# Performance work log

Measured on AMD Instinct MI355X. Metric: run time of the kernel, lower is better.

## Reference

```python
import jax, jax.numpy as jnp
import numpy as np

B, D, K = 32768, 1024, 64
N3, N4, N5 = 512, 512, 512


def setup_inputs() -> dict:
    key = jax.random.key(0)
    ks = jax.random.split(key, 10)
    # x in [-1, 1]^D as the docstring states
    x = jax.random.uniform(ks[0], (B, D), dtype=jnp.float32, minval=-1.0, maxval=1.0)
    S = jnp.sort(jax.random.randint(ks[1], (K,), 0, D, dtype=jnp.int32))
    a = jax.random.normal(ks[2], (K,), dtype=jnp.float32)
    b = jax.random.normal(ks[3], (K, K), dtype=jnp.float32)
    idx3 = jax.random.randint(ks[4], (N3, 3), 0, K, dtype=jnp.int32)
    c3 = jax.random.normal(ks[5], (N3,), dtype=jnp.float32)
    idx4 = jax.random.randint(ks[6], (N4, 4), 0, K, dtype=jnp.int32)
    c4 = jax.random.normal(ks[7], (N4,), dtype=jnp.float32)
    idx5 = jax.random.randint(ks[8], (N5, 5), 0, K, dtype=jnp.int32)
    c5 = jax.random.normal(ks[9], (N5,), dtype=jnp.float32)
    return {"x": x, "S": S, "a": a, "b": b, "idx3": idx3, "c3": c3,
            "idx4": idx4, "c4": c4, "idx5": idx5, "c5": c5}


def _monomial_term(xS, idx, c):
    # xS: (B,k); idx: (n,deg); c: (n,) -> (B,)
    # gather -> (B, n, deg), product over monomial factors, weighted sum
    prod = jnp.prod(xS[:, idx], axis=2)  # (B, n)
    return prod @ c


def reference(x, S, a, b, idx3, c3, idx4, c4, idx5, c5):
    xS = x[:, S]                      # (B, k)
    lin = xS @ a                      # (B,)
    # sum_{i<j} b[i,j] xS_i xS_j == einsum with strictly-upper-triangular b
    bu = jnp.triu(b, k=1)             # (k, k)
    quad = jnp.einsum('bi,ij,bj->b', xS, bu, xS)
    out = lin + quad
    out = out + _monomial_term(xS, idx3, c3)
    out = out + _monomial_term(xS, idx4, c4)
    out = out + _monomial_term(xS, idx5, c5)
    return out
```

## Files before the change

### kernel.cpp

```cpp
#include <hip/hip_runtime.h>
#include <stdint.h>

#define NT 256
#define RPB 16
#define XSTR 80

#define WS_P3   0
#define WS_P4   4096
#define WS_P5   12288
#define WS_BUT  20480

static __device__ __forceinline__ unsigned short f2bf(float f) {
    unsigned u = __float_as_uint(f);
    return (unsigned short)((u + 0x7FFFu + ((u >> 16) & 1u)) >> 16);
}
static __device__ __forceinline__ float bfbits(unsigned lo16) {
    return __uint_as_float(lo16 << 16);
}
static __device__ __forceinline__ float4 f4fma(float s, float4 v, float4 acc) {
    acc.x += s * v.x; acc.y += s * v.y; acc.z += s * v.z; acc.w += s * v.w;
    return acc;
}

__global__ void prepack(const float* __restrict__ b,
                        const int* __restrict__ i3, const float* __restrict__ c3,
                        const int* __restrict__ i4, const float* __restrict__ c4,
                        const int* __restrict__ i5, const float* __restrict__ c5,
                        unsigned char* __restrict__ ws)
{
    const int g = blockIdx.x * NT + threadIdx.x;
    float* buT = (float*)(ws + WS_BUT);
    if (g < 4096) {
        int j = g >> 6, i = g & 63;
        buT[g] = (i < j) ? b[i * 64 + j] : 0.0f;
    }
    if (g < 512) {
        unsigned o0, o1, o2, o3, o4;
        o0 = (unsigned)i3[3*g+0] * XSTR; o1 = (unsigned)i3[3*g+1] * XSTR; o2 = (unsigned)i3[3*g+2] * XSTR;
        ((uint2*)(ws + WS_P3))[g] = make_uint2(o0 | (o1 << 16), o2 | ((unsigned)f2bf(c3[g]) << 16));
        o0 = (unsigned)i4[4*g+0] * XSTR; o1 = (unsigned)i4[4*g+1] * XSTR;
        o2 = (unsigned)i4[4*g+2] * XSTR; o3 = (unsigned)i4[4*g+3] * XSTR;
        ((uint4*)(ws + WS_P4))[g] = make_uint4(o0 | (o1 << 16), o2 | (o3 << 16), (unsigned)f2bf(c4[g]), 0u);
        o0 = (unsigned)i5[5*g+0] * XSTR; o1 = (unsigned)i5[5*g+1] * XSTR;
        o2 = (unsigned)i5[5*g+2] * XSTR; o3 = (unsigned)i5[5*g+3] * XSTR;
        o4 = (unsigned)i5[5*g+4] * XSTR;
        ((uint4*)(ws + WS_P5))[g] = make_uint4(o0 | (o1 << 16), o2 | (o3 << 16), o4 | ((unsigned)f2bf(c5[g]) << 16), 0u);
    }
}

__global__ __launch_bounds__(NT, 4)
void poly_main(const float* __restrict__ x, const int* __restrict__ S,
               const float* __restrict__ a,
               const unsigned char* __restrict__ ws, float* __restrict__ out)
{
    __shared__ __align__(16) float xS[64 * 20];
    __shared__ float red[64];

    const int tid  = threadIdx.x;
    const int row0 = blockIdx.x * RPB;

    {
        const int k = tid & 63, q = tid >> 6;
        const int sk = S[k];
        const float* xc = x + (size_t)row0 * 1024 + sk;
        #pragma unroll
        for (int m = 0; m < 4; ++m) {
            int r = q * 4 + m;
            xS[k * 20 + r] = xc[(size_t)r * 1024];
        }
    }
    __syncthreads();

    const int rg = tid & 3;
    const int ts = tid >> 2;
    const char* xb = (const char*)xS + rg * 16;

    float4 d = make_float4(0.f, 0.f, 0.f, 0.f);
    {
        const float4* buT4 = (const float4*)(ws + WS_BUT) + ts * 16;
        const int nii = (ts + 3) >> 2;
        #pragma unroll 4
        for (int ii = 0; ii < nii; ++ii) {
            float4 bb  = buT4[ii];
            float4 xi0 = *(const float4*)(xb + (ii * 4 + 0) * XSTR);
            float4 xi1 = *(const float4*)(xb + (ii * 4 + 1) * XSTR);
            float4 xi2 = *(const float4*)(xb + (ii * 4 + 2) * XSTR);
            float4 xi3 = *(const float4*)(xb + (ii * 4 + 3) * XSTR);
            d = f4fma(bb.x, xi0, d);
            d = f4fma(bb.y, xi1, d);
            d = f4fma(bb.z, xi2, d);
            d = f4fma(bb.w, xi3, d);
        }
    }
    const float av = a[ts];
    float4 xj = *(const float4*)(xb + ts * XSTR);
    float4 acc;
    acc.x = (av + d.x) * xj.x;
    acc.y = (av + d.y) * xj.y;
    acc.z = (av + d.z) * xj.z;
    acc.w = (av + d.w) * xj.w;

    const uint2* p3 = (const uint2*)(ws + WS_P3);
    const uint4* p4 = (const uint4*)(ws + WS_P4);
    const uint4* p5 = (const uint4*)(ws + WS_P5);

    #pragma unroll 4
    for (int m = 0; m < 8; ++m) {
        uint2 p = p3[64 * m + ts];
        float4 v0 = *(const float4*)(xb + (p.x & 0xFFFFu));
        float4 v1 = *(const float4*)(xb + (p.x >> 16));
        float4 v2 = *(const float4*)(xb + (p.y & 0xFFFFu));
        float c = bfbits(p.y >> 16);
        acc.x += c * ((v0.x * v1.x) * v2.x);
        acc.y += c * ((v0.y * v1.y) * v2.y);
        acc.z += c * ((v0.z * v1.z) * v2.z);
        acc.w += c * ((v0.w * v1.w) * v2.w);
    }
    #pragma unroll 4
    for (int m = 0; m < 8; ++m) {
        uint4 p = p4[64 * m + ts];
        float4 v0 = *(const float4*)(xb + (p.x & 0xFFFFu));
        float4 v1 = *(const float4*)(xb + (p.x >> 16));
        float4 v2 = *(const float4*)(xb + (p.y & 0xFFFFu));
        float4 v3 = *(const float4*)(xb + (p.y >> 16));
        float c = bfbits(p.z & 0xFFFFu);
        acc.x += c * ((v0.x * v1.x) * (v2.x * v3.x));
        acc.y += c * ((v0.y * v1.y) * (v2.y * v3.y));
        acc.z += c * ((v0.z * v1.z) * (v2.z * v3.z));
        acc.w += c * ((v0.w * v1.w) * (v2.w * v3.w));
    }
    #pragma unroll 4
    for (int m = 0; m < 8; ++m) {
        uint4 p = p5[64 * m + ts];
        float4 v0 = *(const float4*)(xb + (p.x & 0xFFFFu));
        float4 v1 = *(const float4*)(xb + (p.x >> 16));
        float4 v2 = *(const float4*)(xb + (p.y & 0xFFFFu));
        float4 v3 = *(const float4*)(xb + (p.y >> 16));
        float4 v4 = *(const float4*)(xb + (p.z & 0xFFFFu));
        float c = bfbits(p.z >> 16);
        acc.x += c * (((v0.x * v1.x) * (v2.x * v3.x)) * v4.x);
        acc.y += c * (((v0.y * v1.y) * (v2.y * v3.y)) * v4.y);
        acc.z += c * (((v0.z * v1.z) * (v2.z * v3.z)) * v4.z);
        acc.w += c * (((v0.w * v1.w) * (v2.w * v3.w)) * v4.w);
    }

    #pragma unroll
    for (int mask = 4; mask <= 32; mask <<= 1) {
        acc.x += __shfl_xor(acc.x, mask, 64);
        acc.y += __shfl_xor(acc.y, mask, 64);
        acc.z += __shfl_xor(acc.z, mask, 64);
        acc.w += __shfl_xor(acc.w, mask, 64);
    }
    const int w = tid >> 6, lane = tid & 63;
    if (lane < 4) ((float4*)red)[w * 4 + lane] = acc;
    __syncthreads();
    if (tid < 16) {
        out[row0 + tid] = red[tid] + red[16 + tid] + red[32 + tid] + red[48 + tid];
    }
}

extern "C" void kernel_launch(void* const* d_in, const int* in_sizes, int n_in,
                              void* d_out, int out_size, void* d_ws, size_t ws_size,
                              hipStream_t stream) {
    const float* x  = (const float*)d_in[0];
    const int*   S  = (const int*)d_in[1];
    const float* a  = (const float*)d_in[2];
    const float* b  = (const float*)d_in[3];
    const int*   i3 = (const int*)d_in[4];
    const float* c3 = (const float*)d_in[5];
    const int*   i4 = (const int*)d_in[6];
    const float* c4 = (const float*)d_in[7];
    const int*   i5 = (const int*)d_in[8];
    const float* c5 = (const float*)d_in[9];
    unsigned char* ws = (unsigned char*)d_ws;
    float* out = (float*)d_out;

    prepack<<<16, NT, 0, stream>>>(b, i3, c3, i4, c4, i5, c5, ws);
    poly_main<<<32768 / RPB, NT, 0, stream>>>(x, S, a, ws, out);
}
```

Measured before the change: 213.3 us.

## Switch gathered features and monomial math to packed fp16 with 32 rows per block

Gathered x values, the triangular b matrix and the monomial coefficients are now stored as fp16, and the quadratic and monomial products are computed with packed half2 FMA/mul, with 8 rows per thread group instead of 4 floats. Rows per block double to 32, so the same LDS row stride holds twice as many rows and each instruction does twice the work. This halves LDS traffic and ALU instruction count per row. The cost is a large precision loss: fp16 accumulation over about 1600 terms with normal-distributed coefficients may overflow or exceed tolerance.

```diff
diff --git a/kernel.cpp b/kernel.cpp
--- a/kernel.cpp
+++ b/kernel.cpp
@@ -1,25 +1,22 @@
 #include <hip/hip_runtime.h>
+#include <hip/hip_fp16.h>
 #include <stdint.h>
 
 #define NT 256
-#define RPB 16
+#define RPB 32
 #define XSTR 80
 
 #define WS_P3   0
 #define WS_P4   4096
 #define WS_P5   12288
-#define WS_BUT  20480
-
-static __device__ __forceinline__ unsigned short f2bf(float f) {
-    unsigned u = __float_as_uint(f);
-    return (unsigned short)((u + 0x7FFFu + ((u >> 16) & 1u)) >> 16);
-}
-static __device__ __forceinline__ float bfbits(unsigned lo16) {
-    return __uint_as_float(lo16 << 16);
-}
-static __device__ __forceinline__ float4 f4fma(float s, float4 v, float4 acc) {
-    acc.x += s * v.x; acc.y += s * v.y; acc.z += s * v.z; acc.w += s * v.w;
-    return acc;
+#define WS_BUTH 20480
+
+static __device__ __forceinline__ __half2 H2(unsigned u) {
+    return __builtin_bit_cast(__half2, u);
+}
+static __device__ __forceinline__ unsigned short f2hbits(float f) {
+    __half h = __float2half(f);
+    return __builtin_bit_cast(unsigned short, h);
 }
 
 __global__ void prepack(const float* __restrict__ b,
@@ -29,23 +26,42 @@
                         unsigned char* __restrict__ ws)
 {
     const int g = blockIdx.x * NT + threadIdx.x;
-    float* buT = (float*)(ws + WS_BUT);
     if (g < 4096) {
         int j = g >> 6, i = g & 63;
-        buT[g] = (i < j) ? b[i * 64 + j] : 0.0f;
+        float v = (i < j) ? b[i * 64 + j] : 0.0f;
+        ((unsigned short*)(ws + WS_BUTH))[g] = f2hbits(v);
     }
     if (g < 512) {
         unsigned o0, o1, o2, o3, o4;
         o0 = (unsigned)i3[3*g+0] * XSTR; o1 = (unsigned)i3[3*g+1] * XSTR; o2 = (unsigned)i3[3*g+2] * XSTR;
-        ((uint2*)(ws + WS_P3))[g] = make_uint2(o0 | (o1 << 16), o2 | ((unsigned)f2bf(c3[g]) << 16));
+        ((uint2*)(ws + WS_P3))[g] = make_uint2(o0 | (o1 << 16), o2 | ((unsigned)f2hbits(c3[g]) << 16));
         o0 = (unsigned)i4[4*g+0] * XSTR; o1 = (unsigned)i4[4*g+1] * XSTR;
         o2 = (unsigned)i4[4*g+2] * XSTR; o3 = (unsigned)i4[4*g+3] * XSTR;
-        ((uint4*)(ws + WS_P4))[g] = make_uint4(o0 | (o1 << 16), o2 | (o3 << 16), (unsigned)f2bf(c4[g]), 0u);
+        ((uint4*)(ws + WS_P4))[g] = make_uint4(o0 | (o1 << 16), o2 | (o3 << 16), (unsigned)f2hbits(c4[g]), 0u);
         o0 = (unsigned)i5[5*g+0] * XSTR; o1 = (unsigned)i5[5*g+1] * XSTR;
         o2 = (unsigned)i5[5*g+2] * XSTR; o3 = (unsigned)i5[5*g+3] * XSTR;
         o4 = (unsigned)i5[5*g+4] * XSTR;
-        ((uint4*)(ws + WS_P5))[g] = make_uint4(o0 | (o1 << 16), o2 | (o3 << 16), o4 | ((unsigned)f2bf(c5[g]) << 16), 0u);
-    }
+        ((uint4*)(ws + WS_P5))[g] = make_uint4(o0 | (o1 << 16), o2 | (o3 << 16), o4 | ((unsigned)f2hbits(c5[g]) << 16), 0u);
+    }
+}
+
+static __device__ __forceinline__ void qfma(__half2 bb, uint4 xk, __half2 d[4]) {
+    d[0] = __hfma2(bb, H2(xk.x), d[0]);
+    d[1] = __hfma2(bb, H2(xk.y), d[1]);
+    d[2] = __hfma2(bb, H2(xk.z), d[2]);
+    d[3] = __hfma2(bb, H2(xk.w), d[3]);
+}
+static __device__ __forceinline__ void pmul(const uint4& a, __half2 p[4]) {
+    p[0] = __hmul2(p[0], H2(a.x));
+    p[1] = __hmul2(p[1], H2(a.y));
+    p[2] = __hmul2(p[2], H2(a.z));
+    p[3] = __hmul2(p[3], H2(a.w));
+}
+static __device__ __forceinline__ void pacc(__half2 c2, const __half2 p[4], __half2 acc[4]) {
+    acc[0] = __hfma2(c2, p[0], acc[0]);
+    acc[1] = __hfma2(c2, p[1], acc[1]);
+    acc[2] = __hfma2(c2, p[2], acc[2]);
+    acc[3] = __hfma2(c2, p[3], acc[3]);
 }
 
 __global__ __launch_bounds__(NT, 4)
@@ -53,8 +69,8 @@
                const float* __restrict__ a,
                const unsigned char* __restrict__ ws, float* __restrict__ out)
 {
-    __shared__ __align__(16) float xS[64 * 20];
-    __shared__ float red[64];
+    __shared__ __align__(16) __half xS[64 * 40];
+    __shared__ float red[4][4][8];
 
     const int tid  = threadIdx.x;
     const int row0 = blockIdx.x * RPB;
@@ -63,11 +79,15 @@
         const int k = tid & 63, q = tid >> 6;
         const int sk = S[k];
         const float* xc = x + (size_t)row0 * 1024 + sk;
+        float v[8];
         #pragma unroll
-        for (int m = 0; m < 4; ++m) {
-            int r = q * 4 + m;
-            xS[k * 20 + r] = xc[(size_t)r * 1024];
-        }
+        for (int m = 0; m < 8; ++m) v[m] = xc[(size_t)(q * 8 + m) * 1024];
+        uint4 pk;
+        pk.x = __builtin_bit_cast(unsigned, __floats2half2_rn(v[0], v[1]));
+        pk.y = __builtin_bit_cast(unsigned, __floats2half2_rn(v[2], v[3]));
+        pk.z = __builtin_bit_cast(unsigned, __floats2half2_rn(v[4], v[5]));
+        pk.w = __builtin_bit_cast(unsigned, __floats2half2_rn(v[6], v[7]));
+        *(uint4*)((char*)xS + k * XSTR + q * 16) = pk;
     }
     __syncthreads();
 
@@ -75,30 +95,35 @@
     const int ts = tid >> 2;
     const char* xb = (const char*)xS + rg * 16;
 
-    float4 d = make_float4(0.f, 0.f, 0.f, 0.f);
+    __half2 d[4] = {H2(0u), H2(0u), H2(0u), H2(0u)};
     {
-        const float4* buT4 = (const float4*)(ws + WS_BUT) + ts * 16;
-        const int nii = (ts + 3) >> 2;
-        #pragma unroll 4
-        for (int ii = 0; ii < nii; ++ii) {
-            float4 bb  = buT4[ii];
-            float4 xi0 = *(const float4*)(xb + (ii * 4 + 0) * XSTR);
-            float4 xi1 = *(const float4*)(xb + (ii * 4 + 1) * XSTR);
-            float4 xi2 = *(const float4*)(xb + (ii * 4 + 2) * XSTR);
-            float4 xi3 = *(const float4*)(xb + (ii * 4 + 3) * XSTR);
-            d = f4fma(bb.x, xi0, d);
-            d = f4fma(bb.y, xi1, d);
-            d = f4fma(bb.z, xi2, d);
-            d = f4fma(bb.w, xi3, d);
+        const uint4* buTh4 = (const uint4*)(ws + WS_BUTH) + ts * 8;
+        const int nii = (ts + 7) >> 3;
+        #pragma unroll 2
+        for (int g = 0; g < nii; ++g) {
+            uint4 bw = buTh4[g];
+            const char* xkb = xb + g * 8 * XSTR;
+            unsigned pw[4] = {bw.x, bw.y, bw.z, bw.w};
+            #pragma unroll
+            for (int p = 0; p < 4; ++p) {
+                __half2 blo = __half2half2(__ushort_as_half((unsigned short)(pw[p] & 0xFFFFu)));
+                __half2 bhi = __half2half2(__ushort_as_half((unsigned short)(pw[p] >> 16)));
+                uint4 x0 = *(const uint4*)(xkb + (2 * p + 0) * XSTR);
+                uint4 x1 = *(const uint4*)(xkb + (2 * p + 1) * XSTR);
+                qfma(blo, x0, d);
+                qfma(bhi, x1, d);
+            }
         }
     }
-    const float av = a[ts];
-    float4 xj = *(const float4*)(xb + ts * XSTR);
-    float4 acc;
-    acc.x = (av + d.x) * xj.x;
-    acc.y = (av + d.y) * xj.y;
-    acc.z = (av + d.z) * xj.z;
-    acc.w = (av + d.w) * xj.w;
+    __half2 acc[4];
+    {
+        __half2 a2 = __half2half2(__float2half(a[ts]));
+        uint4 xj = *(const uint4*)(xb + ts * XSTR);
+        acc[0] = __hmul2(__hadd2(a2, d[0]), H2(xj.x));
+        acc[1] = __hmul2(__hadd2(a2, d[1]), H2(xj.y));
+        acc[2] = __hmul2(__hadd2(a2, d[2]), H2(xj.z));
+        acc[3] = __hmul2(__hadd2(a2, d[3]), H2(xj.w));
+    }
 
     const uint2* p3 = (const uint2*)(ws + WS_P3);
     const uint4* p4 = (const uint4*)(ws + WS_P4);
@@ -107,55 +132,63 @@
     #pragma unroll 4
     for (int m = 0; m < 8; ++m) {
         uint2 p = p3[64 * m + ts];
-        float4 v0 = *(const float4*)(xb + (p.x & 0xFFFFu));
-        float4 v1 = *(const float4*)(xb + (p.x >> 16));
-        float4 v2 = *(const float4*)(xb + (p.y & 0xFFFFu));
-        float c = bfbits(p.y >> 16);
-        acc.x += c * ((v0.x * v1.x) * v2.x);
-        acc.y += c * ((v0.y * v1.y) * v2.y);
-        acc.z += c * ((v0.z * v1.z) * v2.z);
-        acc.w += c * ((v0.w * v1.w) * v2.w);
-    }
-    #pragma unroll 4
+        uint4 v0 = *(const uint4*)(xb + (p.x & 0xFFFFu));
+        uint4 v1 = *(const uint4*)(xb + (p.x >> 16));
+        uint4 v2 = *(const uint4*)(xb + (p.y & 0xFFFFu));
+        __half2 pr[4] = {H2(v0.x), H2(v0.y), H2(v0.z), H2(v0.w)};
+        pmul(v1, pr);
+        pmul(v2, pr);
+        pacc(__half2half2(__ushort_as_half((unsigned short)(p.y >> 16))), pr, acc);
+    }
+    #pragma unroll 2
     for (int m = 0; m < 8; ++m) {
         uint4 p = p4[64 * m + ts];
-        float4 v0 = *(const float4*)(xb + (p.x & 0xFFFFu));
-        float4 v1 = *(const float4*)(xb + (p.x >> 16));
-        float4 v2 = *(const float4*)(xb + (p.y & 0xFFFFu));
-        float4 v3 = *(const float4*)(xb + (p.y >> 16));
-        float c = bfbits(p.z & 0xFFFFu);
-        acc.x += c * ((v0.x * v1.x) * (v2.x * v3.x));
-        acc.y += c * ((v0.y * v1.y) * (v2.y * v3.y));
-        acc.z += c * ((v0.z * v1.z) * (v2.z * v3.z));
-        acc.w += c * ((v0.w * v1.w) * (v2.w * v3.w));
-    }
-    #pragma unroll 4
+        uint4 v0 = *(const uint4*)(xb + (p.x & 0xFFFFu));
+        uint4 v1 = *(const uint4*)(xb + (p.x >> 16));
+        uint4 v2 = *(const uint4*)(xb + (p.y & 0xFFFFu));
+        uint4 v3 = *(const uint4*)(xb + (p.y >> 16));
+        __half2 pr[4] = {H2(v0.x), H2(v0.y), H2(v0.z), H2(v0.w)};
+        pmul(v1, pr);
+        pmul(v2, pr);
+        pmul(v3, pr);
+        pacc(__half2half2(__ushort_as_half((unsigned short)(p.z & 0xFFFFu))), pr, acc);
+    }
+    #pragma unroll 2
     for (int m = 0; m < 8; ++m) {
         uint4 p = p5[64 * m + ts];
-        float4 v0 = *(const float4*)(xb + (p.x & 0xFFFFu));
-        float4 v1 = *(const float4*)(xb + (p.x >> 16));
-        float4 v2 = *(const float4*)(xb + (p.y & 0xFFFFu));
-        float4 v3 = *(const float4*)(xb + (p.y >> 16));
-        float4 v4 = *(const float4*)(xb + (p.z & 0xFFFFu));
-        float c = bfbits(p.z >> 16);
-        acc.x += c * (((v0.x * v1.x) * (v2.x * v3.x)) * v4.x);
-        acc.y += c * (((v0.y * v1.y) * (v2.y * v3.y)) * v4.y);
-        acc.z += c * (((v0.z * v1.z) * (v2.z * v3.z)) * v4.z);
-        acc.w += c * (((v0.w * v1.w) * (v2.w * v3.w)) * v4.w);
-    }
-
+        uint4 v0 = *(const uint4*)(xb + (p.x & 0xFFFFu));
+        uint4 v1 = *(const uint4*)(xb + (p.x >> 16));
+        uint4 v2 = *(const uint4*)(xb + (p.y & 0xFFFFu));
+        uint4 v3 = *(const uint4*)(xb + (p.y >> 16));
+        uint4 v4 = *(const uint4*)(xb + (p.z & 0xFFFFu));
+        __half2 pr[4] = {H2(v0.x), H2(v0.y), H2(v0.z), H2(v0.w)};
+        pmul(v1, pr);
+        pmul(v2, pr);
+        pmul(v3, pr);
+        pmul(v4, pr);
+        pacc(__half2half2(__ushort_as_half((unsigned short)(p.z >> 16))), pr, acc);
+    }
+
+    float f[8];
+    #pragma unroll
+    for (int e = 0; e < 4; ++e) {
+        f[2 * e]     = __low2float(acc[e]);
+        f[2 * e + 1] = __high2float(acc[e]);
+    }
     #pragma unroll
     for (int mask = 4; mask <= 32; mask <<= 1) {
-        acc.x += __shfl_xor(acc.x, mask, 64);
-        acc.y += __shfl_xor(acc.y, mask, 64);
-        acc.z += __shfl_xor(acc.z, mask, 64);
-        acc.w += __shfl_xor(acc.w, mask, 64);
+        #pragma unroll
+        for (int r = 0; r < 8; ++r) f[r] += __shfl_xor(f[r], mask, 64);
     }
     const int w = tid >> 6, lane = tid & 63;
-    if (lane < 4) ((float4*)red)[w * 4 + lane] = acc;
+    if (lane < 4) {
+        #pragma unroll
+        for (int r = 0; r < 8; ++r) red[w][lane][r] = f[r];
+    }
     __syncthreads();
-    if (tid < 16) {
-        out[row0 + tid] = red[tid] + red[16 + tid] + red[32 + tid] + red[48 + tid];
+    if (tid < 32) {
+        int g = tid >> 3, e = tid & 7;
+        out[row0 + tid] = red[0][g][e] + red[1][g][e] + red[2][g][e] + red[3][g][e];
     }
 }
 
```

Measured after the change: 210.1 us. No clear change (-1.5%).
